# Kernel tuning notes

Hardware: AMD Instinct MI355X
Metric: run time of the kernel (lower is better)

The kernel has to match this reference:

```python
import jax, jax.numpy as jnp
import numpy as np

D_MODEL = 512
N_HEADS = 8
D_K = D_MODEL // N_HEADS


def setup_inputs() -> dict:
    key = jax.random.key(0)
    ks = jax.random.split(key, 7)
    s = 1.0 / np.sqrt(D_MODEL)
    return {
        "x": jax.random.normal(ks[0], (2, 4096, D_MODEL), dtype=jnp.float32),
        "W_q": jax.random.normal(ks[1], (D_MODEL, D_MODEL), dtype=jnp.float32) * s,
        "W_k": jax.random.normal(ks[2], (D_MODEL, D_MODEL), dtype=jnp.float32) * s,
        "W_v": jax.random.normal(ks[3], (D_MODEL, D_MODEL), dtype=jnp.float32) * s,
        "b_v": jax.random.normal(ks[4], (D_MODEL,), dtype=jnp.float32) * s,
        "W_o": jax.random.normal(ks[5], (D_MODEL, D_MODEL), dtype=jnp.float32) * s,
        "b_o": jax.random.normal(ks[6], (D_MODEL,), dtype=jnp.float32) * s,
    }


def _split_heads(t):
    # [N, S, d_model] -> [N, H, S, d_k]
    N, S, _ = t.shape
    return t.reshape(N, S, N_HEADS, D_K).transpose(0, 2, 1, 3)


def reference(x, W_q, W_k, W_v, b_v, W_o, b_o):
    N, S, _ = x.shape
    # nn.Linear computes x @ W.T (+ b)
    Q = _split_heads(x @ W_q.T)
    K = _split_heads(x @ W_k.T)
    V = _split_heads(x @ W_v.T + b_v)
    scale = jnp.sqrt(jnp.asarray(D_K, x.dtype))
    scores = jnp.einsum('nhqd,nhkd->nhqk', Q, K) / scale  # [N,H,S,S]
    causal = jnp.tril(jnp.ones((S, S), dtype=bool))
    scores = jnp.where(causal, scores, -jnp.inf)
    attn = jax.nn.softmax(scores, axis=-1)
    out = jnp.einsum('nhqk,nhkd->nhqd', attn, V)  # [N,H,S,d_k]
    out = out.transpose(0, 2, 1, 3).reshape(N, S, D_MODEL)
    return out @ W_o.T + b_o
```

## Files before the change

### kernel.cpp

```cpp
#include <hip/hip_runtime.h>
#include <hip/hip_bf16.h>

#define NB 2
#define SEQ 4096
#define DM 512
#define NH 8
#define DKH 64
#define MTOT (NB*SEQ)

typedef __attribute__((ext_vector_type(4))) float f32x4;
typedef __attribute__((ext_vector_type(16))) float f32x16;
typedef __attribute__((ext_vector_type(8))) short bf16x8;
typedef __attribute__((ext_vector_type(2))) unsigned uint2v;

__device__ inline unsigned short f2bf(float f) {
    union { float f; unsigned int u; } v; v.f = f;
    unsigned int r = v.u + 0x7FFFu + ((v.u >> 16) & 1u);
    return (unsigned short)(r >> 16);
}

#define QSCALE 0.18033688011112042f

__global__ void cast_kernel(const float* __restrict__ x, const float* __restrict__ wq,
                            const float* __restrict__ wk, const float* __restrict__ wv,
                            const float* __restrict__ wo, unsigned short* __restrict__ dst) {
    const int NX = MTOT*DM;
    const int NW = DM*DM;
    int i4 = blockIdx.x * blockDim.x + threadIdx.x;
    long e = (long)i4 * 4;
    if (e >= NX + 4L*NW) return;
    const float* src; long off;
    if (e < NX)           { src = x;  off = e; }
    else if (e < NX+NW)   { src = wq; off = e - NX; }
    else if (e < NX+2*NW) { src = wk; off = e - NX - NW; }
    else if (e < NX+3*NW) { src = wv; off = e - NX - 2*NW; }
    else                  { src = wo; off = e - NX - 3*NW; }
    float4 v = *reinterpret_cast<const float4*>(src + off);
    ushort4 o;
    o.x = f2bf(v.x); o.y = f2bf(v.y); o.z = f2bf(v.z); o.w = f2bf(v.w);
    *reinterpret_cast<ushort4*>(dst + e) = o;
}

#define GEMM_KLOOP(BROW, BCOL)                                                     \
    f32x4 acc[4][4] = {};                                                          \
    for (int kt = 0; kt < 8; ++kt) {                                               \
        __syncthreads();                                                           \
        _Pragma("unroll")                                                          \
        for (int i = 0; i < 4; ++i) {                                              \
            int rbase = i*32 + wid*8;                                              \
            int row = rbase + (lane >> 3);                                         \
            int csrc = (lane & 7) ^ (row & 7);                                     \
            const unsigned short* asrc = Aptr_ + (long)((BROW)+row)*512 + kt*64 + csrc*8; \
            __builtin_amdgcn_global_load_lds(                                      \
                (const __attribute__((address_space(1))) unsigned int*)asrc,       \
                (__attribute__((address_space(3))) unsigned int*)&As[rbase*64], 16, 0, 0); \
            const unsigned short* bsrc = Bptr_ + (long)((BCOL)+row)*512 + kt*64 + csrc*8; \
            __builtin_amdgcn_global_load_lds(                                      \
                (const __attribute__((address_space(1))) unsigned int*)bsrc,       \
                (__attribute__((address_space(3))) unsigned int*)&Bs[rbase*64], 16, 0, 0); \
        }                                                                          \
        __syncthreads();                                                           \
        _Pragma("unroll")                                                          \
        for (int kk = 0; kk < 2; ++kk) {                                           \
            bf16x8 af[4], bfr[4];                                                  \
            _Pragma("unroll")                                                      \
            for (int mi = 0; mi < 4; ++mi) {                                       \
                int row = wr*64 + mi*16 + l15;                                     \
                int colb = (kk*32 + l4*8) * 2;                                     \
                af[mi] = *reinterpret_cast<const bf16x8*>(                         \
                    reinterpret_cast<const char*>(As) + row*128 + (colb ^ ((row&7)<<4))); \
            }                                                                      \
            _Pragma("unroll")                                                      \
            for (int ni = 0; ni < 4; ++ni) {                                       \
                int row = wc*64 + ni*16 + l15;                                     \
                int colb = (kk*32 + l4*8) * 2;                                     \
                bfr[ni] = *reinterpret_cast<const bf16x8*>(                        \
                    reinterpret_cast<const char*>(Bs) + row*128 + (colb ^ ((row&7)<<4))); \
            }                                                                      \
            _Pragma("unroll")                                                      \
            for (int mi = 0; mi < 4; ++mi)                                         \
                _Pragma("unroll")                                                  \
                for (int ni = 0; ni < 4; ++ni)                                     \
                    acc[mi][ni] = __builtin_amdgcn_mfma_f32_16x16x32_bf16(af[mi], bfr[ni], acc[mi][ni], 0, 0, 0); \
        }                                                                          \
    }

__global__ __launch_bounds__(256, 2) void gemm_qkv(
    const unsigned short* __restrict__ A,
    const unsigned short* __restrict__ B,
    const float* __restrict__ bv,
    unsigned short* __restrict__ Qh, unsigned short* __restrict__ Kh,
    unsigned short* __restrict__ Vt)
{
    __shared__ __align__(16) unsigned short As[128*64];
    __shared__ __align__(16) unsigned short Bs[128*64];
    __shared__ __align__(16) unsigned short Trs[64*136];
    int tid = threadIdx.x;
    int wid = tid >> 6, lane = tid & 63;
    int wr = wid >> 1, wc = wid & 1;
    int brow = blockIdx.x * 128;
    int by   = blockIdx.y;
    int bcol = by * 128;
    int l15 = lane & 15, l4 = lane >> 4;
    const unsigned short* Aptr_ = A;
    const unsigned short* Bptr_ = B;

    GEMM_KLOOP(brow, bcol)

    if (by < 8) {
        #pragma unroll
        for (int mi = 0; mi < 4; ++mi) {
            #pragma unroll
            for (int ni = 0; ni < 4; ++ni) {
                #pragma unroll
                for (int r = 0; r < 4; ++r) {
                    int row = brow + wr*64 + mi*16 + l4*4 + r;
                    int col = bcol + wc*64 + ni*16 + l15;
                    float v = acc[mi][ni][r];
                    int which = col >> 9;
                    int cw = col & 511;
                    int h = cw >> 6, d = cw & 63;
                    int b = row >> 12, s = row & 4095;
                    int bh = b*NH + h;
                    if (which == 0)
                        Qh[((long)(bh*SEQ + s))*DKH + d] = f2bf(v * QSCALE);
                    else
                        Kh[((long)(bh*SEQ + s))*DKH + d] = f2bf(v);
                }
            }
        }
    } else {
        const int b = brow >> 12;
        const int stile = brow & 4095;
        #pragma unroll 1
        for (int hs = 0; hs < 2; ++hs) {
            __syncthreads();
            if (wc == hs) {
                #pragma unroll
                for (int mi = 0; mi < 4; ++mi) {
                    #pragma unroll
                    for (int ni = 0; ni < 4; ++ni) {
                        #pragma unroll
                        for (int r = 0; r < 4; ++r) {
                            int rowLoc = wr*64 + mi*16 + l4*4 + r;
                            int colH = ni*16 + l15;
                            int cw = (bcol + hs*64 + colH) & 511;
                            Trs[colH*136 + rowLoc] = f2bf(acc[mi][ni][r] + bv[cw]);
                        }
                    }
                }
            }
            __syncthreads();
            #pragma unroll
            for (int pass = 0; pass < 4; ++pass) {
                int idx = pass*256 + tid;
                int dd = idx >> 4;
                int s8 = (idx & 15) << 3;
                bf16x8 vv = *reinterpret_cast<const bf16x8*>(&Trs[dd*136 + s8]);
                int cw = ((bcol - 1024) + hs*64 + dd);
                int h = cw >> 6, d = cw & 63;
                int bh = b*NH + h;
                *reinterpret_cast<bf16x8*>(Vt + ((long)(bh*DKH + d))*SEQ + stile + s8) = vv;
            }
        }
    }
}

__global__ __launch_bounds__(256, 2) void gemm_out(
    const unsigned short* __restrict__ A,
    const unsigned short* __restrict__ B,
    const float* __restrict__ bias, float* __restrict__ Cout)
{
    __shared__ __align__(16) unsigned short As[128*64];
    __shared__ __align__(16) unsigned short Bs[128*64];
    int tid = threadIdx.x;
    int wid = tid >> 6, lane = tid & 63;
    int wr = wid >> 1, wc = wid & 1;
    int brow = blockIdx.x * 128;
    int bcol = blockIdx.y * 128;
    int l15 = lane & 15, l4 = lane >> 4;
    const unsigned short* Aptr_ = A;
    const unsigned short* Bptr_ = B;

    GEMM_KLOOP(brow, bcol)

    #pragma unroll
    for (int mi = 0; mi < 4; ++mi) {
        #pragma unroll
        for (int ni = 0; ni < 4; ++ni) {
            #pragma unroll
            for (int r = 0; r < 4; ++r) {
                int row = brow + wr*64 + mi*16 + l4*4 + r;
                int col = bcol + wc*64 + ni*16 + l15;
                Cout[(long)row*DM + col] = acc[mi][ni][r] + bias[col];
            }
        }
    }
}

#define PV_STEP_M(SV, VLS, KS, B0, OD0, OD1, LS)  do {                             \
        unsigned c0, c1, c2, c3;                                                   \
        float t0 = SV[B0+0], t1 = SV[B0+1], t2 = SV[B0+2], t3 = SV[B0+3];          \
        float t4 = SV[B0+4], t5 = SV[B0+5], t6 = SV[B0+6], t7 = SV[B0+7];          \
        asm("v_cvt_pk_bf16_f32 %0, %1, %2" : "=v"(c0) : "v"(t0), "v"(t1));         \
        asm("v_cvt_pk_bf16_f32 %0, %1, %2" : "=v"(c1) : "v"(t2), "v"(t3));         \
        asm("v_cvt_pk_bf16_f32 %0, %1, %2" : "=v"(c2) : "v"(t4), "v"(t5));         \
        asm("v_cvt_pk_bf16_f32 %0, %1, %2" : "=v"(c3) : "v"(t6), "v"(t7));         \
        uint2v sw0 = __builtin_amdgcn_permlane32_swap(c0, c2, false, false);       \
        uint2v sw1 = __builtin_amdgcn_permlane32_swap(c1, c3, false, false);       \
        union { unsigned u[4]; bf16x8 v; } pu;                                     \
        pu.u[0] = sw0[0]; pu.u[1] = sw1[0]; pu.u[2] = sw0[1]; pu.u[3] = sw1[1];    \
        bf16x8 vf0 = *reinterpret_cast<const bf16x8*>(VLS + l31*128      + (((KS)*32 + hi*16) ^ swz)); \
        OD0 = __builtin_amdgcn_mfma_f32_32x32x16_bf16(vf0, pu.v, OD0, 0, 0, 0);    \
        bf16x8 vf1 = *reinterpret_cast<const bf16x8*>(VLS + (32+l31)*128 + (((KS)*32 + hi*16) ^ swz)); \
        OD1 = __builtin_amdgcn_mfma_f32_32x32x16_bf16(vf1, pu.v, OD1, 0, 0, 0);    \
        LS  = __builtin_amdgcn_mfma_f32_32x32x16_bf16(onesv, pu.v, LS, 0, 0, 0);   \
    } while (0)

__global__ __launch_bounds__(256, 4) void attn_fm(
    const unsigned short* __restrict__ Qh,
    const unsigned short* __restrict__ Kh,
    const unsigned short* __restrict__ Vt,
    unsigned short* __restrict__ Obf)
{
    __shared__ __align__(16) unsigned short Kc[2][64*64];
    __shared__ __align__(16) unsigned short Vc[2][64*64];
    const int tid = threadIdx.x;
    const int wid = tid >> 6, lane = tid & 63;
    const int g = wid & 1, p = wid >> 1;
    const int l31 = lane & 31;
    const int hi  = lane >> 5;

    const int id   = blockIdx.x;
    const int xcd  = id & 7;
    const int rest = id >> 3;
    const int bh   = xcd + ((rest & 1) << 3);
    const int t    = 63 - (rest >> 1);

    const unsigned short* Qbase = Qh + (long)bh*SEQ*DKH;
    const unsigned short* Kbase = Kh + (long)bh*SEQ*DKH;
    const unsigned short* Vbase = Vt + (long)bh*DKH*SEQ;

    const int q0w = t*64 + g*32;
    const int q   = q0w + l31;
    const int nu  = t + 1;
    const int swz = (l31 & 7) << 4;

    bf16x8 qf[4];
    #pragma unroll
    for (int kk = 0; kk < 4; ++kk)
        qf[kk] = *reinterpret_cast<const bf16x8*>(Qbase + (long)q*DKH + kk*16 + hi*8);

    bf16x8 onesv;
    #pragma unroll
    for (int e = 0; e < 8; ++e) onesv[e] = (short)0x3F80;

    auto STAGE = [&](int b, int key0) {
        #pragma unroll
        for (int ii = 0; ii < 2; ++ii) {
            const int rbase = wid*16 + ii*8;
            const int row = rbase + (lane >> 3);
            const int ck = (lane & 7) ^ (row & 7);
            const unsigned short* ksrc = Kbase + (long)(key0 + row)*DKH + ck*8;
            __builtin_amdgcn_global_load_lds(
                (const __attribute__((address_space(1))) unsigned int*)ksrc,
                (__attribute__((address_space(3))) unsigned int*)&Kc[b][rbase*64], 16, 0, 0);
            const unsigned short* vsrc = Vbase + (long)row*SEQ + key0 + ck*8;
            __builtin_amdgcn_global_load_lds(
                (const __attribute__((address_space(1))) unsigned int*)vsrc,
                (__attribute__((address_space(3))) unsigned int*)&Vc[b][rbase*64], 16, 0, 0);
        }
    };

    f32x16 od0 = {}, od1 = {}, ls = {};

    STAGE(0, 0);
    __syncthreads();
    int cur = 0;

    #pragma unroll 1
    for (int u = 0; u < nu; ++u) {
        if (u + 1 < nu) STAGE(cur ^ 1, (u + 1) << 6);
        const char* kl = reinterpret_cast<const char*>(&Kc[cur][0]) + p*32*128;
        const char* vl = reinterpret_cast<const char*>(&Vc[cur][0]);

        bf16x8 kfr[4];
        #pragma unroll
        for (int kk = 0; kk < 4; ++kk)
            kfr[kk] = *reinterpret_cast<const bf16x8*>(kl + l31*128 + ((kk*32 + hi*16) ^ swz));
        f32x16 sv = {};
        __builtin_amdgcn_s_setprio(1);
        #pragma unroll
        for (int kk = 0; kk < 4; ++kk)
            sv = __builtin_amdgcn_mfma_f32_32x32x16_bf16(kfr[kk], qf[kk], sv, 0, 0, 0);
        __builtin_amdgcn_s_setprio(0);

        if (u == t) {
            const int kbase = (u << 6) + (p << 5);
            #pragma unroll
            for (int r = 0; r < 16; ++r) {
                const int ko = (r&3) + 8*(r>>2) + 4*hi;
                if (kbase + ko > q) sv[r] = -1e30f;
            }
        }

        #pragma unroll
        for (int r = 0; r < 16; ++r)
            sv[r] = __builtin_amdgcn_exp2f(sv[r]);

        __builtin_amdgcn_s_setprio(1);
        PV_STEP_M(sv, vl, (2*p),     0, od0, od1, ls);
        PV_STEP_M(sv, vl, (2*p + 1), 8, od0, od1, ls);
        __builtin_amdgcn_s_setprio(0);

        __syncthreads();
        cur ^= 1;
    }

    float lsum = ls[0];
    char*  sod = reinterpret_cast<char*>(&Kc[g][0]);
    float* sml = reinterpret_cast<float*>(&Vc[g][0]);
    const int lswz = (lane & 7) << 4;
    if (p == 1) {
        #pragma unroll
        for (int i = 0; i < 4; ++i) {
            *reinterpret_cast<f32x4*>(sod + lane*128 + ((i*16) ^ lswz)) =
                (f32x4){od0[i*4+0], od0[i*4+1], od0[i*4+2], od0[i*4+3]};
            *reinterpret_cast<f32x4*>(sod + lane*128 + (((i+4)*16) ^ lswz)) =
                (f32x4){od1[i*4+0], od1[i*4+1], od1[i*4+2], od1[i*4+3]};
        }
        sml[lane] = lsum;
    }
    __syncthreads();
    if (p == 0) {
        lsum += sml[lane];
        #pragma unroll
        for (int i = 0; i < 4; ++i) {
            f32x4 t0 = *reinterpret_cast<const f32x4*>(sod + lane*128 + ((i*16) ^ lswz));
            f32x4 t1 = *reinterpret_cast<const f32x4*>(sod + lane*128 + (((i+4)*16) ^ lswz));
            #pragma unroll
            for (int k = 0; k < 4; ++k) {
                od0[i*4+k] += t0[k];
                od1[i*4+k] += t1[k];
            }
        }
        const float rls = 1.0f / lsum;
        const long obase = (long)((bh >> 3)*SEQ + q)*DM + (bh & 7)*DKH;
        #pragma unroll
        for (int rr = 0; rr < 4; ++rr) {
            ushort4 w0, w1;
            w0.x = f2bf(od0[rr*4+0]*rls); w0.y = f2bf(od0[rr*4+1]*rls);
            w0.z = f2bf(od0[rr*4+2]*rls); w0.w = f2bf(od0[rr*4+3]*rls);
            *reinterpret_cast<ushort4*>(Obf + obase + rr*8 + hi*4) = w0;
            w1.x = f2bf(od1[rr*4+0]*rls); w1.y = f2bf(od1[rr*4+1]*rls);
            w1.z = f2bf(od1[rr*4+2]*rls); w1.w = f2bf(od1[rr*4+3]*rls);
            *reinterpret_cast<ushort4*>(Obf + obase + 32 + rr*8 + hi*4) = w1;
        }
    }
}

extern "C" void kernel_launch(void* const* d_in, const int* in_sizes, int n_in,
                              void* d_out, int out_size, void* d_ws, size_t ws_size,
                              hipStream_t stream) {
    const float* x  = (const float*)d_in[0];
    const float* wq = (const float*)d_in[1];
    const float* wk = (const float*)d_in[2];
    const float* wv = (const float*)d_in[3];
    const float* bv = (const float*)d_in[4];
    const float* wo = (const float*)d_in[5];
    const float* bo = (const float*)d_in[6];
    float* out = (float*)d_out;

    unsigned short* ws = (unsigned short*)d_ws;
    unsigned short* Xbf  = ws;
    unsigned short* Wqkv = Xbf  + 4194304;
    unsigned short* Wob  = Wqkv + 786432;
    unsigned short* Qh   = Wob  + 262144;
    unsigned short* Kh   = Qh   + 4194304;
    unsigned short* Vt   = Kh   + 4194304;
    unsigned short* Obf  = Vt   + 4194304;

    cast_kernel<<<5120, 256, 0, stream>>>(x, wq, wk, wv, wo, Xbf);

    dim3 gqkv(64, 12);
    gemm_qkv<<<gqkv, 256, 0, stream>>>(Xbf, Wqkv, bv, Qh, Kh, Vt);

    attn_fm<<<1024, 256, 0, stream>>>(Qh, Kh, Vt, Obf);

    dim3 go(64, 4);
    gemm_out<<<go, 256, 0, stream>>>(Obf, Wob, bo, out);
}
```

Baseline: 98.10 us.

## Pair causal query tiles per block and split 128-key tiles across 8 waves

The attention kernel now runs 512 blocks of 512 threads. Each block processes two query tiles, j and 63-j, so every block gets the same amount of causal work and the tail imbalance across CUs shrinks. Each iteration stages a 128-key chunk of K and V, split four ways across wave pairs, and a wider LDS reduction combines the four partial outputs and row sums. The costs are doubled LDS per block (64KB), which caps blocks per CU, some wasted masked work on the final 128-key chunk, and extra barriers for the reduction.

```diff
diff --git a/kernel.cpp b/kernel.cpp
--- a/kernel.cpp
+++ b/kernel.cpp
@@ -217,17 +217,17 @@
         LS  = __builtin_amdgcn_mfma_f32_32x32x16_bf16(onesv, pu.v, LS, 0, 0, 0);   \
     } while (0)
 
-__global__ __launch_bounds__(256, 4) void attn_fm(
+__global__ __launch_bounds__(512, 4) void attn_fm(
     const unsigned short* __restrict__ Qh,
     const unsigned short* __restrict__ Kh,
     const unsigned short* __restrict__ Vt,
     unsigned short* __restrict__ Obf)
 {
-    __shared__ __align__(16) unsigned short Kc[2][64*64];
-    __shared__ __align__(16) unsigned short Vc[2][64*64];
+    __shared__ __align__(16) unsigned short Kc[2][128*64];
+    __shared__ __align__(16) unsigned short Vc[2][2][64*64];
     const int tid = threadIdx.x;
     const int wid = tid >> 6, lane = tid & 63;
-    const int g = wid & 1, p = wid >> 1;
+    const int g = wid & 1, s = wid >> 1;
     const int l31 = lane & 31;
     const int hi  = lane >> 5;
 
@@ -235,21 +235,12 @@
     const int xcd  = id & 7;
     const int rest = id >> 3;
     const int bh   = xcd + ((rest & 1) << 3);
-    const int t    = 63 - (rest >> 1);
+    const int j    = rest >> 1;
 
     const unsigned short* Qbase = Qh + (long)bh*SEQ*DKH;
     const unsigned short* Kbase = Kh + (long)bh*SEQ*DKH;
     const unsigned short* Vbase = Vt + (long)bh*DKH*SEQ;
-
-    const int q0w = t*64 + g*32;
-    const int q   = q0w + l31;
-    const int nu  = t + 1;
     const int swz = (l31 & 7) << 4;
-
-    bf16x8 qf[4];
-    #pragma unroll
-    for (int kk = 0; kk < 4; ++kk)
-        qf[kk] = *reinterpret_cast<const bf16x8*>(Qbase + (long)q*DKH + kk*16 + hi*8);
 
     bf16x8 onesv;
     #pragma unroll
@@ -259,103 +250,127 @@
         #pragma unroll
         for (int ii = 0; ii < 2; ++ii) {
             const int rbase = wid*16 + ii*8;
-            const int row = rbase + (lane >> 3);
-            const int ck = (lane & 7) ^ (row & 7);
-            const unsigned short* ksrc = Kbase + (long)(key0 + row)*DKH + ck*8;
+            const int krow = rbase + (lane >> 3);
+            const int ck = (lane & 7) ^ (krow & 7);
+            const unsigned short* ksrc = Kbase + (long)(key0 + krow)*DKH + ck*8;
             __builtin_amdgcn_global_load_lds(
                 (const __attribute__((address_space(1))) unsigned int*)ksrc,
                 (__attribute__((address_space(3))) unsigned int*)&Kc[b][rbase*64], 16, 0, 0);
-            const unsigned short* vsrc = Vbase + (long)row*SEQ + key0 + ck*8;
+            const int jj = rbase >> 6;
+            const int dbase = rbase & 63;
+            const int drow = dbase + (lane >> 3);
+            const int cv = (lane & 7) ^ (drow & 7);
+            const unsigned short* vsrc = Vbase + (long)drow*SEQ + key0 + jj*64 + cv*8;
             __builtin_amdgcn_global_load_lds(
                 (const __attribute__((address_space(1))) unsigned int*)vsrc,
-                (__attribute__((address_space(3))) unsigned int*)&Vc[b][rbase*64], 16, 0, 0);
+                (__attribute__((address_space(3))) unsigned int*)&Vc[b][jj][dbase*64], 16, 0, 0);
         }
     };
 
-    f32x16 od0 = {}, od1 = {}, ls = {};
-
-    STAGE(0, 0);
-    __syncthreads();
-    int cur = 0;
-
     #pragma unroll 1
-    for (int u = 0; u < nu; ++u) {
-        if (u + 1 < nu) STAGE(cur ^ 1, (u + 1) << 6);
-        const char* kl = reinterpret_cast<const char*>(&Kc[cur][0]) + p*32*128;
-        const char* vl = reinterpret_cast<const char*>(&Vc[cur][0]);
-
-        bf16x8 kfr[4];
+    for (int tt = 0; tt < 2; ++tt) {
+        const int T  = tt ? j : 63 - j;
+        const int q  = T*64 + g*32 + l31;
+        const int nu = (T >> 1) + 1;
+
+        bf16x8 qf[4];
         #pragma unroll
         for (int kk = 0; kk < 4; ++kk)
-            kfr[kk] = *reinterpret_cast<const bf16x8*>(kl + l31*128 + ((kk*32 + hi*16) ^ swz));
-        f32x16 sv = {};
-        __builtin_amdgcn_s_setprio(1);
-        #pragma unroll
-        for (int kk = 0; kk < 4; ++kk)
-            sv = __builtin_amdgcn_mfma_f32_32x32x16_bf16(kfr[kk], qf[kk], sv, 0, 0, 0);
-        __builtin_amdgcn_s_setprio(0);
-
-        if (u == t) {
-            const int kbase = (u << 6) + (p << 5);
-            #pragma unroll
-            for (int r = 0; r < 16; ++r) {
-                const int ko = (r&3) + 8*(r>>2) + 4*hi;
-                if (kbase + ko > q) sv[r] = -1e30f;
-            }
-        }
-
-        #pragma unroll
-        for (int r = 0; r < 16; ++r)
-            sv[r] = __builtin_amdgcn_exp2f(sv[r]);
-
-        __builtin_amdgcn_s_setprio(1);
-        PV_STEP_M(sv, vl, (2*p),     0, od0, od1, ls);
-        PV_STEP_M(sv, vl, (2*p + 1), 8, od0, od1, ls);
-        __builtin_amdgcn_s_setprio(0);
-
+            qf[kk] = *reinterpret_cast<const bf16x8*>(Qbase + (long)q*DKH + kk*16 + hi*8);
+
+        f32x16 od0 = {}, od1 = {}, ls = {};
+
+        STAGE(0, 0);
         __syncthreads();
-        cur ^= 1;
-    }
-
-    float lsum = ls[0];
-    char*  sod = reinterpret_cast<char*>(&Kc[g][0]);
-    float* sml = reinterpret_cast<float*>(&Vc[g][0]);
-    const int lswz = (lane & 7) << 4;
-    if (p == 1) {
-        #pragma unroll
-        for (int i = 0; i < 4; ++i) {
-            *reinterpret_cast<f32x4*>(sod + lane*128 + ((i*16) ^ lswz)) =
-                (f32x4){od0[i*4+0], od0[i*4+1], od0[i*4+2], od0[i*4+3]};
-            *reinterpret_cast<f32x4*>(sod + lane*128 + (((i+4)*16) ^ lswz)) =
-                (f32x4){od1[i*4+0], od1[i*4+1], od1[i*4+2], od1[i*4+3]};
-        }
-        sml[lane] = lsum;
-    }
-    __syncthreads();
-    if (p == 0) {
-        lsum += sml[lane];
-        #pragma unroll
-        for (int i = 0; i < 4; ++i) {
-            f32x4 t0 = *reinterpret_cast<const f32x4*>(sod + lane*128 + ((i*16) ^ lswz));
-            f32x4 t1 = *reinterpret_cast<const f32x4*>(sod + lane*128 + (((i+4)*16) ^ lswz));
-            #pragma unroll
-            for (int k = 0; k < 4; ++k) {
-                od0[i*4+k] += t0[k];
-                od1[i*4+k] += t1[k];
-            }
-        }
-        const float rls = 1.0f / lsum;
-        const long obase = (long)((bh >> 3)*SEQ + q)*DM + (bh & 7)*DKH;
-        #pragma unroll
-        for (int rr = 0; rr < 4; ++rr) {
-            ushort4 w0, w1;
-            w0.x = f2bf(od0[rr*4+0]*rls); w0.y = f2bf(od0[rr*4+1]*rls);
-            w0.z = f2bf(od0[rr*4+2]*rls); w0.w = f2bf(od0[rr*4+3]*rls);
-            *reinterpret_cast<ushort4*>(Obf + obase + rr*8 + hi*4) = w0;
-            w1.x = f2bf(od1[rr*4+0]*rls); w1.y = f2bf(od1[rr*4+1]*rls);
-            w1.z = f2bf(od1[rr*4+2]*rls); w1.w = f2bf(od1[rr*4+3]*rls);
-            *reinterpret_cast<ushort4*>(Obf + obase + 32 + rr*8 + hi*4) = w1;
-        }
+        int cur = 0;
+
+        #pragma unroll 1
+        for (int u = 0; u < nu; ++u) {
+            if (u + 1 < nu) STAGE(cur ^ 1, (u + 1) << 7);
+
+            const char* kl = reinterpret_cast<const char*>(&Kc[cur][0]) + s*32*128;
+            const char* vl = reinterpret_cast<const char*>(&Vc[cur][s >> 1][0]);
+            const int hh = s & 1;
+
+            bf16x8 kfr[4];
+            #pragma unroll
+            for (int kk = 0; kk < 4; ++kk)
+                kfr[kk] = *reinterpret_cast<const bf16x8*>(kl + l31*128 + ((kk*32 + hi*16) ^ swz));
+            f32x16 sv = {};
+            __builtin_amdgcn_s_setprio(1);
+            #pragma unroll
+            for (int kk = 0; kk < 4; ++kk)
+                sv = __builtin_amdgcn_mfma_f32_32x32x16_bf16(kfr[kk], qf[kk], sv, 0, 0, 0);
+            __builtin_amdgcn_s_setprio(0);
+
+            if (u == nu - 1) {
+                const int kbase = (u << 7) + (s << 5);
+                #pragma unroll
+                for (int r = 0; r < 16; ++r) {
+                    const int ko = kbase + (r&3) + 8*(r>>2) + 4*hi;
+                    if (ko > q) sv[r] = -1e30f;
+                }
+            }
+
+            #pragma unroll
+            for (int r = 0; r < 16; ++r)
+                sv[r] = __builtin_amdgcn_exp2f(sv[r]);
+
+            __builtin_amdgcn_s_setprio(1);
+            PV_STEP_M(sv, vl, (2*hh),     0, od0, od1, ls);
+            PV_STEP_M(sv, vl, (2*hh + 1), 8, od0, od1, ls);
+            __builtin_amdgcn_s_setprio(0);
+
+            __syncthreads();
+            cur ^= 1;
+        }
+
+        float lsum = ls[0];
+        char* lbase = reinterpret_cast<char*>(&Kc[0][0]);
+        float* sml = reinterpret_cast<float*>(lbase + 49152);
+        const int lswz = (lane & 7) << 4;
+        if (s != 0) {
+            char* d = lbase + (g*3 + s - 1)*8192;
+            #pragma unroll
+            for (int i = 0; i < 4; ++i) {
+                *reinterpret_cast<f32x4*>(d + lane*128 + ((i*16) ^ lswz)) =
+                    (f32x4){od0[i*4+0], od0[i*4+1], od0[i*4+2], od0[i*4+3]};
+                *reinterpret_cast<f32x4*>(d + lane*128 + (((i+4)*16) ^ lswz)) =
+                    (f32x4){od1[i*4+0], od1[i*4+1], od1[i*4+2], od1[i*4+3]};
+            }
+            sml[(g*3 + s - 1)*64 + lane] = lsum;
+        }
+        __syncthreads();
+        if (s == 0) {
+            #pragma unroll 1
+            for (int w = 1; w <= 3; ++w) {
+                const char* d = lbase + (g*3 + w - 1)*8192;
+                lsum += sml[(g*3 + w - 1)*64 + lane];
+                #pragma unroll
+                for (int i = 0; i < 4; ++i) {
+                    f32x4 t0 = *reinterpret_cast<const f32x4*>(d + lane*128 + ((i*16) ^ lswz));
+                    f32x4 t1 = *reinterpret_cast<const f32x4*>(d + lane*128 + (((i+4)*16) ^ lswz));
+                    #pragma unroll
+                    for (int k = 0; k < 4; ++k) {
+                        od0[i*4+k] += t0[k];
+                        od1[i*4+k] += t1[k];
+                    }
+                }
+            }
+            const float rls = 1.0f / lsum;
+            const long obase = (long)((bh >> 3)*SEQ + q)*DM + (bh & 7)*DKH;
+            #pragma unroll
+            for (int rr = 0; rr < 4; ++rr) {
+                ushort4 w0, w1;
+                w0.x = f2bf(od0[rr*4+0]*rls); w0.y = f2bf(od0[rr*4+1]*rls);
+                w0.z = f2bf(od0[rr*4+2]*rls); w0.w = f2bf(od0[rr*4+3]*rls);
+                *reinterpret_cast<ushort4*>(Obf + obase + rr*8 + hi*4) = w0;
+                w1.x = f2bf(od1[rr*4+0]*rls); w1.y = f2bf(od1[rr*4+1]*rls);
+                w1.z = f2bf(od1[rr*4+2]*rls); w1.w = f2bf(od1[rr*4+3]*rls);
+                *reinterpret_cast<ushort4*>(Obf + obase + 32 + rr*8 + hi*4) = w1;
+            }
+        }
+        __syncthreads();
     }
 }
 
@@ -385,7 +400,7 @@
     dim3 gqkv(64, 12);
     gemm_qkv<<<gqkv, 256, 0, stream>>>(Xbf, Wqkv, bv, Qh, Kh, Vt);
 
-    attn_fm<<<1024, 256, 0, stream>>>(Qh, Kh, Vt, Obf);
+    attn_fm<<<512, 512, 0, stream>>>(Qh, Kh, Vt, Obf);
 
     dim3 go(64, 4);
     gemm_out<<<go, 256, 0, stream>>>(Obf, Wob, bo, out);
```

New measurement: 97.90 us. No clear change (-0.2%).
